# Performance work log

Hardware: AMD Instinct MI355X
Metric: run time of the kernel (lower is better)

The kernel has to match this reference:

```python
import jax, jax.numpy as jnp
import numpy as np

N_NODES = 10000
N_EDGES = 50000
IN_F = 1433
OUT_F = 256
EPSILON = 8.0
SENSITIVITY = 1.0
DELTA = 1e-5
# total noise = sum of 3 independent per-share Gaussian draws
SIGMA = np.sqrt(3.0) * np.sqrt(2.0 * np.log(1.25 / DELTA)) * SENSITIVITY / EPSILON


def setup_inputs() -> dict:
    key = jax.random.key(0)
    k1, k2, k3, k4, k5, k6 = jax.random.split(key, 6)
    input_features = jax.random.normal(k1, (N_NODES, IN_F), dtype=jnp.float32)
    dst = jax.random.randint(k2, (N_EDGES,), 0, N_NODES)
    # src in [0, N_NODES]; value == N_NODES is the zero-vector sentinel
    src = jax.random.randint(k3, (N_EDGES,), 0, N_NODES + 1)
    edges = jnp.stack([dst, src], axis=1).astype(jnp.int64)
    stdv = 1.0 / np.sqrt(OUT_F)
    weight = jax.random.uniform(k4, (IN_F, OUT_F), minval=-stdv, maxval=stdv, dtype=jnp.float32)
    bias = jax.random.uniform(k5, (OUT_F,), minval=-stdv, maxval=stdv, dtype=jnp.float32)
    noise = jax.random.normal(k6, (N_NODES, IN_F), dtype=jnp.float32) * jnp.float32(SIGMA)
    return {"input_features": input_features, "edges": edges, "weight": weight,
            "bias": bias, "noise": noise}


def reference(input_features, edges, weight, bias, noise):
    n = input_features.shape[0]
    dst = edges[:, 0]
    src = edges[:, 1]
    # gather per-edge source features; sentinel src == n -> zero vector
    valid = (src < n)[:, None]                                   # [E,1]
    gathered = jnp.where(valid, input_features[jnp.clip(src, 0, n - 1)], 0.0)  # [E,F]
    # three secret shares sum exactly back to the value; the per-key aggregation
    # of each share then summed equals a single segment-sum over destinations
    agg = jax.ops.segment_sum(gathered, dst, num_segments=n)      # [N,F]
    # DP noise added to each share -> total noise added to the sum
    agg = agg + noise
    # torch.nn.functional.normalize(p=2, dim=1) with eps=1e-12
    norm = jnp.maximum(jnp.linalg.norm(agg, axis=1, keepdims=True), 1e-12)
    normed = agg / norm
    return normed @ weight + bias
```

## Files before the change

kernel.cpp:

```cpp
#include <hip/hip_runtime.h>
#include <math.h>

#define N_NODES 10000
#define N_EDGES 50000
#define IN_F    1433
#define OUT_F   256
#define GK      1440
#define NCHUNK  180
#define GM2     10112
#define CAP     32

typedef __bf16 bf16x8 __attribute__((ext_vector_type(8)));
typedef float  f32x4  __attribute__((ext_vector_type(4)));

typedef __attribute__((address_space(3))) unsigned int lds_u32;
typedef __attribute__((address_space(1))) unsigned int glb_u32;

__device__ __forceinline__ void stage16(const void* g, void* l) {
    __builtin_amdgcn_global_load_lds((glb_u32*)g, (lds_u32*)l, 16, 0, 0);
}


#define PREP_W      (OUT_F * GK)
#define FILL_BLKS   ((N_EDGES + 255) / 256)
#define CONV_BLKS   (N_NODES / 4)
#define PREP_BLKS   (PREP_W / 256)
#define PHASEA_BLKS (FILL_BLKS + CONV_BLKS + PREP_BLKS)

__global__ void __launch_bounds__(256) k_phaseA(const float* __restrict__ X,
                                                __bf16* __restrict__ Xbf,
                                                const float* __restrict__ W,
                                                __bf16* __restrict__ BT,
                                                const int* __restrict__ edges,
                                                int* __restrict__ cnt,
                                                int* __restrict__ slots,
                                                int* __restrict__ ovf) {
    const int t = threadIdx.x;
    const int b = blockIdx.x;

    if (b < FILL_BLKS) {
        int e = b * 256 + t;
        if (e < N_EDGES) {
            int dst = edges[2 * e];
            int src = edges[2 * e + 1];
            if ((unsigned)src < N_NODES) {
                int pos = atomicAdd(&cnt[dst], 1);
                if (pos < CAP) {
                    slots[dst * CAP + pos] = src;
                } else {
                    int o = atomicAdd(&cnt[N_NODES], 1);
                    ovf[2 * o]     = dst;
                    ovf[2 * o + 1] = src;
                }
            }
        }
        return;
    }

    if (b < FILL_BLKS + CONV_BLKS) {
        const int w = t >> 6, lane = t & 63;
        const int r = (b - FILL_BLKS) * 4 + w;
        const size_t rowf = (size_t)r * IN_F;
        __bf16* orow = Xbf + (size_t)r * GK;
        const int d = r & 3;

        f32x4 A[3][3];
#pragma unroll
        for (int s2 = 0; s2 < 3; ++s2) {
            int k = lane + s2 * 64;
            int kc = (k > 178) ? 178 : k;
            size_t q0 = (rowf + (size_t)kc * 8) >> 2;
            A[s2][0] = ((const f32x4*)X)[q0];
            A[s2][1] = ((const f32x4*)X)[q0 + 1];
            A[s2][2] = ((const f32x4*)X)[q0 + 2];
        }

#pragma unroll
        for (int s2 = 0; s2 < 3; ++s2) {
            int k = lane + s2 * 64;
            float q[12];
            *(f32x4*)&q[0] = A[s2][0];
            *(f32x4*)&q[4] = A[s2][1];
            *(f32x4*)&q[8] = A[s2][2];
            if (k < 179) {
                bf16x8 v;
                switch (d) {
                case 0:
#pragma unroll
                    for (int j = 0; j < 8; ++j) v[j] = (__bf16)q[0 + j];
                    break;
                case 1:
#pragma unroll
                    for (int j = 0; j < 8; ++j) v[j] = (__bf16)q[1 + j];
                    break;
                case 2:
#pragma unroll
                    for (int j = 0; j < 8; ++j) v[j] = (__bf16)q[2 + j];
                    break;
                default:
#pragma unroll
                    for (int j = 0; j < 8; ++j) v[j] = (__bf16)q[3 + j];
                    break;
                }
                *(bf16x8*)(orow + k * 8) = v;
            } else if (k == 179) {
                bf16x8 v;
                v[0] = (__bf16)q[8 + d];
#pragma unroll
                for (int j = 1; j < 8; ++j) v[j] = (__bf16)0.0f;
                *(bf16x8*)(orow + 1432) = v;
            }
        }
        return;
    }

    {
        int i = (b - FILL_BLKS - CONV_BLKS) * 256 + t;
        int n = i / GK, k = i % GK;
        BT[i] = (__bf16)((k < IN_F) ? W[(size_t)k * OUT_F + n] : 0.0f);
    }
}


__global__ void __launch_bounds__(192) k_agg(const __bf16* __restrict__ Xbf,
                                             const float* __restrict__ noise,
                                             const int* __restrict__ cnt,
                                             const int* __restrict__ slots,
                                             const int* __restrict__ ovf,
                                             __bf16* __restrict__ aggbf,
                                             float* __restrict__ rnorm) {
    __shared__ float red[3];
    const int node = blockIdx.x;
    const int t = threadIdx.x;
    const bool active = (t < NCHUNK);
    const size_t co = (size_t)t * 8;

    if (node >= N_NODES) {
        if (active) {
            bf16x8 z;
#pragma unroll
            for (int j = 0; j < 8; ++j) z[j] = (__bf16)0.0f;
            *(bf16x8*)(aggbf + (size_t)node * GK + co) = z;
        }
        return;
    }

    const size_t nrowf = (size_t)node * IN_F;
    const int d = node & 3;
    f32x4 na, nb, nc;
    if (active) {
        int kc = (t > 178) ? 178 : t;
        size_t q0 = (nrowf + (size_t)kc * 8) >> 2;
        na = ((const f32x4*)noise)[q0];
        nb = ((const f32x4*)noise)[q0 + 1];
        nc = ((const f32x4*)noise)[q0 + 2];
    }

    const int cn = cnt[node];
    const int ns = (cn < CAP) ? cn : CAP;
    const int* sl = slots + node * CAP;

    float acc[8] = {0.f, 0.f, 0.f, 0.f, 0.f, 0.f, 0.f, 0.f};

    int kk = 0;
    for (; kk + 3 < ns; kk += 4) {
        int n0 = sl[kk], n1 = sl[kk + 1];
        int n2 = sl[kk + 2], n3 = sl[kk + 3];
        if (active) {
            bf16x8 v0 = *(const bf16x8*)(Xbf + (size_t)n0 * GK + co);
            bf16x8 v1 = *(const bf16x8*)(Xbf + (size_t)n1 * GK + co);
            bf16x8 v2 = *(const bf16x8*)(Xbf + (size_t)n2 * GK + co);
            bf16x8 v3 = *(const bf16x8*)(Xbf + (size_t)n3 * GK + co);
#pragma unroll
            for (int j = 0; j < 8; ++j)
                acc[j] += ((float)v0[j] + (float)v1[j]) + ((float)v2[j] + (float)v3[j]);
        }
    }
    for (; kk < ns; ++kk) {
        int n0 = sl[kk];
        if (active) {
            bf16x8 v = *(const bf16x8*)(Xbf + (size_t)n0 * GK + co);
#pragma unroll
            for (int j = 0; j < 8; ++j) acc[j] += (float)v[j];
        }
    }

    if (cn > CAP) {
        const int L = cnt[N_NODES];
        for (int i = 0; i < L; ++i) {
            if (ovf[2 * i] == node) {
                int n0 = ovf[2 * i + 1];
                if (active) {
                    bf16x8 v = *(const bf16x8*)(Xbf + (size_t)n0 * GK + co);
#pragma unroll
                    for (int j = 0; j < 8; ++j) acc[j] += (float)v[j];
                }
            }
        }
    }

    if (active) {
        float nq[12];
        *(f32x4*)&nq[0] = na; *(f32x4*)&nq[4] = nb; *(f32x4*)&nq[8] = nc;
        if (t < 179) {
            switch (d) {
            case 0:
#pragma unroll
                for (int j = 0; j < 8; ++j) acc[j] += nq[0 + j];
                break;
            case 1:
#pragma unroll
                for (int j = 0; j < 8; ++j) acc[j] += nq[1 + j];
                break;
            case 2:
#pragma unroll
                for (int j = 0; j < 8; ++j) acc[j] += nq[2 + j];
                break;
            default:
#pragma unroll
                for (int j = 0; j < 8; ++j) acc[j] += nq[3 + j];
                break;
            }
        } else {
            acc[0] += nq[8 + d];
        }
    }

    float ss = 0.f;
    if (active) {
        bf16x8 o;
#pragma unroll
        for (int j = 0; j < 8; ++j) { o[j] = (__bf16)acc[j]; ss += acc[j] * acc[j]; }
        *(bf16x8*)(aggbf + (size_t)node * GK + co) = o;
    }
    for (int off = 32; off > 0; off >>= 1) ss += __shfl_down(ss, off, 64);
    if ((t & 63) == 0) red[t >> 6] = ss;
    __syncthreads();
    if (t == 0)
        rnorm[node] = 1.0f / fmaxf(sqrtf(red[0] + red[1] + red[2]), 1e-12f);
}


#define BK 32
#define GEMM_NWG ((GM2 / 128) * (OUT_F / 64))

__global__ void __launch_bounds__(256) k_gemm(const __bf16* __restrict__ A,
                                              const __bf16* __restrict__ BT,
                                              const float* __restrict__ rnorm,
                                              const float* __restrict__ bias,
                                              float* __restrict__ out) {
    __shared__ __align__(16) __bf16 Asm[128][BK];
    __shared__ __align__(16) __bf16 Bsm[64][BK];

    const int t = threadIdx.x;
    const int lane = t & 63;
    const int w = t >> 6;

    const int L   = blockIdx.x;
    const int xcd = L & 7, idx = L >> 3;
    const int q = GEMM_NWG >> 3, r = GEMM_NWG & 7;
    const int work = (xcd < r) ? xcd * (q + 1) + idx
                               : r * (q + 1) + (xcd - r) * q + idx;
    const int row0 = (work >> 2) * 128;
    const int col0 = (work & 3) * 64;

    const int sm = t >> 2;
    const int sc = (t & 3) * 8;

    f32x4 acc[2][4];
#pragma unroll
    for (int i = 0; i < 2; ++i)
#pragma unroll
        for (int j = 0; j < 4; ++j) acc[i][j] = (f32x4){0.f, 0.f, 0.f, 0.f};

    __bf16* asm0 = (__bf16*)Asm;
    __bf16* bsm0 = (__bf16*)Bsm;

#pragma unroll
    for (int rr = 0; rr < 2; ++rr)
        stage16(A + (size_t)(row0 + sm + rr * 64) * GK + sc, asm0 + rr * 2048 + t * 8);
    stage16(BT + (size_t)(col0 + sm) * GK + sc, bsm0 + t * 8);

    const int kq = (lane >> 4) * 8;
    const int l15 = lane & 15;

    for (int kt = 0; kt < GK / BK; ++kt) {
        __syncthreads();

        bf16x8 af[2], bfr[4];
#pragma unroll
        for (int i = 0; i < 2; ++i) af[i]  = *(const bf16x8*)&Asm[w * 32 + i * 16 + l15][kq];
#pragma unroll
        for (int j = 0; j < 4; ++j) bfr[j] = *(const bf16x8*)&Bsm[j * 16 + l15][kq];

        __syncthreads();

        if (kt + 1 < GK / BK) {
            int k0 = (kt + 1) * BK;
#pragma unroll
            for (int rr = 0; rr < 2; ++rr)
                stage16(A + (size_t)(row0 + sm + rr * 64) * GK + k0 + sc, asm0 + rr * 2048 + t * 8);
            stage16(BT + (size_t)(col0 + sm) * GK + k0 + sc, bsm0 + t * 8);
        }

#pragma unroll
        for (int i = 0; i < 2; ++i)
#pragma unroll
            for (int j = 0; j < 4; ++j)
                acc[i][j] = __builtin_amdgcn_mfma_f32_16x16x32_bf16(af[i], bfr[j], acc[i][j], 0, 0, 0);
    }

    const int rq4 = (lane >> 4) * 4;
#pragma unroll
    for (int i = 0; i < 2; ++i) {
        int gr0 = row0 + w * 32 + i * 16 + rq4;
#pragma unroll
        for (int rr = 0; rr < 4; ++rr) {
            int gr = gr0 + rr;
            if (gr < N_NODES) {
                float rn = rnorm[gr];
#pragma unroll
                for (int j = 0; j < 4; ++j) {
                    int gc = col0 + j * 16 + l15;
                    out[(size_t)gr * OUT_F + gc] = acc[i][j][rr] * rn + bias[gc];
                }
            }
        }
    }
}


extern "C" void kernel_launch(void* const* d_in, const int* in_sizes, int n_in,
                              void* d_out, int out_size, void* d_ws, size_t ws_size,
                              hipStream_t stream) {
    const float* feat  = (const float*)d_in[0];
    const int*   edges = (const int*)d_in[1];
    const float* W     = (const float*)d_in[2];
    const float* bias  = (const float*)d_in[3];
    const float* noise = (const float*)d_in[4];
    float* out = (float*)d_out;

    char* ws = (char*)d_ws;
    size_t off = 0;
    auto carve = [&](size_t bytes) {
        void* p = ws + off;
        off = (off + bytes + 255) & ~(size_t)255;
        return p;
    };
    __bf16* Xbf     = (__bf16*)carve((size_t)N_NODES * GK * sizeof(__bf16));
    __bf16* aggbf   = (__bf16*)carve((size_t)GM2 * GK * sizeof(__bf16));
    __bf16* WbfT    = (__bf16*)carve((size_t)OUT_F * GK * sizeof(__bf16));
    float*  rnorm   = (float*)carve((size_t)N_NODES * sizeof(float));
    int*    cnt     = (int*)carve((size_t)(N_NODES + 1) * sizeof(int));
    int*    slots   = (int*)carve((size_t)N_NODES * CAP * sizeof(int));
    int*    ovf     = (int*)carve((size_t)2 * N_EDGES * sizeof(int));
    (void)ws_size;

    hipMemsetAsync(cnt, 0, (size_t)(N_NODES + 1) * sizeof(int), stream);

    k_phaseA<<<PHASEA_BLKS, 256, 0, stream>>>(feat, Xbf, W, WbfT,
                                              edges, cnt, slots, ovf);

    k_agg<<<GM2, 192, 0, stream>>>(Xbf, noise, cnt, slots, ovf, aggbf, rnorm);

    k_gemm<<<GEMM_NWG, 256, 0, stream>>>(aggbf, WbfT, rnorm, bias, out);
}
```

Before: 193.6 us.

## Retile GEMM to 64x64 tiles with deeper K and transpose weights via LDS

The weight transpose/convert now goes through an LDS tile: each block reads 16 rows of W with coalesced vector loads and writes bf16x8 vectors into the transposed BT, replacing the strided per-element gather. The GEMM changes from 128x64 tiles with K-step 32 to 64x64 tiles with K-step 96 and a 2x2 wave layout. This doubles the workgroup count for occupancy and cuts the number of barrier-separated K iterations. The cost is more LDS traffic per MFMA and half the accumulator reuse per wave.

```diff
diff --git a/kernel.cpp b/kernel.cpp
--- a/kernel.cpp
+++ b/kernel.cpp
@@ -21,10 +21,9 @@
 }
 
 
-#define PREP_W      (OUT_F * GK)
 #define FILL_BLKS   ((N_EDGES + 255) / 256)
 #define CONV_BLKS   (N_NODES / 4)
-#define PREP_BLKS   (PREP_W / 256)
+#define PREP_BLKS   (GK / 16)
 #define PHASEA_BLKS (FILL_BLKS + CONV_BLKS + PREP_BLKS)
 
 __global__ void __launch_bounds__(256) k_phaseA(const float* __restrict__ X,
@@ -35,6 +34,7 @@
                                                 int* __restrict__ cnt,
                                                 int* __restrict__ slots,
                                                 int* __restrict__ ovf) {
+    __shared__ float wt[16][256];
     const int t = threadIdx.x;
     const int b = blockIdx.x;
 
@@ -115,9 +115,24 @@
     }
 
     {
-        int i = (b - FILL_BLKS - CONV_BLKS) * 256 + t;
-        int n = i / GK, k = i % GK;
-        BT[i] = (__bf16)((k < IN_F) ? W[(size_t)k * OUT_F + n] : 0.0f);
+        const int bp = b - FILL_BLKS - CONV_BLKS;
+        const int k0 = bp * 16;
+#pragma unroll
+        for (int g2 = 0; g2 < 4; ++g2) {
+            int g = t + g2 * 256;
+            int r = g >> 6, c4 = g & 63;
+            int krow = k0 + r;
+            f32x4 v = (krow < IN_F)
+                        ? ((const f32x4*)(W + (size_t)krow * OUT_F))[c4]
+                        : (f32x4){0.f, 0.f, 0.f, 0.f};
+            *(f32x4*)&wt[r][c4 * 4] = v;
+        }
+        __syncthreads();
+        bf16x8 o0, o1;
+#pragma unroll
+        for (int r = 0; r < 8; ++r) { o0[r] = (__bf16)wt[r][t]; o1[r] = (__bf16)wt[8 + r][t]; }
+        *(bf16x8*)(BT + (size_t)t * GK + k0)     = o0;
+        *(bf16x8*)(BT + (size_t)t * GK + k0 + 8) = o1;
     }
 }
 
@@ -241,87 +256,90 @@
 }
 
 
-#define BK 32
-#define GEMM_NWG ((GM2 / 128) * (OUT_F / 64))
+#define BKG 96
+#define GEMM_NWG ((GM2 / 64) * (OUT_F / 64))
 
 __global__ void __launch_bounds__(256) k_gemm(const __bf16* __restrict__ A,
                                               const __bf16* __restrict__ BT,
                                               const float* __restrict__ rnorm,
                                               const float* __restrict__ bias,
                                               float* __restrict__ out) {
-    __shared__ __align__(16) __bf16 Asm[128][BK];
-    __shared__ __align__(16) __bf16 Bsm[64][BK];
+    __shared__ __align__(16) __bf16 Asm[64][BKG];
+    __shared__ __align__(16) __bf16 Bsm[64][BKG];
 
     const int t = threadIdx.x;
     const int lane = t & 63;
     const int w = t >> 6;
-
-    const int L   = blockIdx.x;
+    const int wr = w >> 1, wc = w & 1;
+
+    const int L = blockIdx.x;
     const int xcd = L & 7, idx = L >> 3;
-    const int q = GEMM_NWG >> 3, r = GEMM_NWG & 7;
-    const int work = (xcd < r) ? xcd * (q + 1) + idx
-                               : r * (q + 1) + (xcd - r) * q + idx;
-    const int row0 = (work >> 2) * 128;
+    const int work = xcd * (GEMM_NWG / 8) + idx;
+    const int row0 = (work >> 2) * 64;
     const int col0 = (work & 3) * 64;
 
-    const int sm = t >> 2;
-    const int sc = (t & 3) * 8;
-
-    f32x4 acc[2][4];
+    f32x4 acc[2][2];
 #pragma unroll
     for (int i = 0; i < 2; ++i)
 #pragma unroll
-        for (int j = 0; j < 4; ++j) acc[i][j] = (f32x4){0.f, 0.f, 0.f, 0.f};
+        for (int j = 0; j < 2; ++j) acc[i][j] = (f32x4){0.f, 0.f, 0.f, 0.f};
 
     __bf16* asm0 = (__bf16*)Asm;
     __bf16* bsm0 = (__bf16*)Bsm;
 
-#pragma unroll
-    for (int rr = 0; rr < 2; ++rr)
-        stage16(A + (size_t)(row0 + sm + rr * 64) * GK + sc, asm0 + rr * 2048 + t * 8);
-    stage16(BT + (size_t)(col0 + sm) * GK + sc, bsm0 + t * 8);
+    auto stage_tile = [&](int k0) {
+#pragma unroll
+        for (int g2 = 0; g2 < 3; ++g2) {
+            int g = t + g2 * 256;
+            int r = g / 12, c16 = g % 12;
+            stage16(A  + (size_t)(row0 + r) * GK + k0 + c16 * 8, asm0 + g * 8);
+            stage16(BT + (size_t)(col0 + r) * GK + k0 + c16 * 8, bsm0 + g * 8);
+        }
+    };
+
+    stage_tile(0);
 
     const int kq = (lane >> 4) * 8;
     const int l15 = lane & 15;
 
-    for (int kt = 0; kt < GK / BK; ++kt) {
+    for (int kt = 0; kt < GK / BKG; ++kt) {
         __syncthreads();
 
-        bf16x8 af[2], bfr[4];
-#pragma unroll
-        for (int i = 0; i < 2; ++i) af[i]  = *(const bf16x8*)&Asm[w * 32 + i * 16 + l15][kq];
-#pragma unroll
-        for (int j = 0; j < 4; ++j) bfr[j] = *(const bf16x8*)&Bsm[j * 16 + l15][kq];
+        bf16x8 af[2][3], bfr[2][3];
+#pragma unroll
+        for (int s = 0; s < 3; ++s) {
+#pragma unroll
+            for (int i = 0; i < 2; ++i) {
+                af[i][s]  = *(const bf16x8*)&Asm[wr * 32 + i * 16 + l15][s * 32 + kq];
+                bfr[i][s] = *(const bf16x8*)&Bsm[wc * 32 + i * 16 + l15][s * 32 + kq];
+            }
+        }
 
         __syncthreads();
 
-        if (kt + 1 < GK / BK) {
-            int k0 = (kt + 1) * BK;
-#pragma unroll
-            for (int rr = 0; rr < 2; ++rr)
-                stage16(A + (size_t)(row0 + sm + rr * 64) * GK + k0 + sc, asm0 + rr * 2048 + t * 8);
-            stage16(BT + (size_t)(col0 + sm) * GK + k0 + sc, bsm0 + t * 8);
-        }
-
-#pragma unroll
-        for (int i = 0; i < 2; ++i)
-#pragma unroll
-            for (int j = 0; j < 4; ++j)
-                acc[i][j] = __builtin_amdgcn_mfma_f32_16x16x32_bf16(af[i], bfr[j], acc[i][j], 0, 0, 0);
+        if (kt + 1 < GK / BKG) stage_tile((kt + 1) * BKG);
+
+#pragma unroll
+        for (int s = 0; s < 3; ++s)
+#pragma unroll
+            for (int i = 0; i < 2; ++i)
+#pragma unroll
+                for (int j = 0; j < 2; ++j)
+                    acc[i][j] = __builtin_amdgcn_mfma_f32_16x16x32_bf16(af[i][s], bfr[j][s], acc[i][j], 0, 0, 0);
     }
 
     const int rq4 = (lane >> 4) * 4;
 #pragma unroll
     for (int i = 0; i < 2; ++i) {
-        int gr0 = row0 + w * 32 + i * 16 + rq4;
+        int gr0 = row0 + wr * 32 + i * 16 + rq4;
 #pragma unroll
         for (int rr = 0; rr < 4; ++rr) {
             int gr = gr0 + rr;
             if (gr < N_NODES) {
                 float rn = rnorm[gr];
 #pragma unroll
-                for (int j = 0; j < 4; ++j) {
-                    int gc = col0 + j * 16 + l15;
+                for (int j = 0; j < 2; ++j) {
+                    int gc = col0 + wc * 32 + j * 16 + l15;
                     out[(size_t)gr * OUT_F + gc] = acc[i][j][rr] * rn + bias[gc];
                 }
             }
```

Result: faster. 184.0 us (-5.0%).
